# Kernel tuning notes

Measured on AMD Instinct MI355X. Metric: run time of the kernel, lower is better.

## Reference

```python
import jax, jax.numpy as jnp
import numpy as np

HIDDEN = 768
B = 32
GRID_X, GRID_Y = 84, 30          # 84*30 = 2520 input patches
SEQ = GRID_X * GRID_Y            # 2520
OUT_LEN = 280                    # 2520 // 280 = 9 -> k = 3


def setup_inputs() -> dict:
    key = jax.random.key(0)
    k1, k2 = jax.random.split(key)
    hidden_states = jax.random.normal(k1, (B, SEQ, HIDDEN), dtype=jnp.float32)
    # (x, y) grid coordinates for each patch, identical across batch
    x = jnp.arange(SEQ, dtype=jnp.int32) % GRID_X
    y = jnp.arange(SEQ, dtype=jnp.int32) // GRID_X
    pos = jnp.stack([x, y], axis=-1)                     # [SEQ, 2]
    pixel_position_ids = jnp.broadcast_to(pos, (B, SEQ, 2))
    padding_positions = jax.random.bernoulli(k2, 0.05, (B, SEQ))  # bool mask
    return {
        "hidden_states": hidden_states,
        "pixel_position_ids": pixel_position_ids,
        "padding_positions": padding_positions,
        "output_length": OUT_LEN,
    }


def reference(hidden_states, pixel_position_ids, padding_positions, output_length):
    root_hidden_size = hidden_states.shape[-1] ** 0.5
    # zero out padded patches
    hs = jnp.where(padding_positions[..., None], 0.0, hidden_states)
    seq_len = hs.shape[1]
    if seq_len != output_length:
        k = int((seq_len // output_length) ** 0.5)
        k_squared = k * k
        clamped = jnp.maximum(pixel_position_ids, 0)            # [B, S, 2]
        max_x = jnp.max(clamped[..., 0], axis=-1, keepdims=True) + 1  # [B, 1]
        kidx = clamped // k
        seg = kidx[..., 0] + (max_x // k) * kidx[..., 1]        # [B, S] bucket ids
        hs32 = hs.astype(jnp.float32)
        # segment-sum per batch == one_hot(seg).T @ hs, without the dense one-hot
        pooled = jax.vmap(
            lambda h, i: jax.ops.segment_sum(h, i, num_segments=output_length)
        )(hs32, seg) / k_squared                                 # [B, L, H]
        counts = jax.vmap(
            lambda i: jax.ops.segment_sum(jnp.ones_like(i), i, num_segments=output_length)
        )(seg)                                                   # [B, L]
        mask = counts > 0  # bucket received at least one patch (one-hot col nonzero)
        hs = pooled.astype(hidden_states.dtype)
        padding_positions = mask
    hs = hs * root_hidden_size
    return hs, padding_positions
```

## Files before the change

kernel.cpp:

```cpp
#include <hip/hip_runtime.h>
#include <math.h>


#define NB    32
#define SEQL  2520
#define HID   768
#define OUTL  280
#define CAP   16
#define GX    84
#define KP    3
#define MXK   (GX / KP)

typedef float f32x4 __attribute__((ext_vector_type(4)));

__global__ void __launch_bounds__(256)
k_verify(const int* __restrict__ pos, const int* __restrict__ padding,
         int* __restrict__ flags, int* __restrict__ ents,
         float* __restrict__ out_mask) {
    __shared__ int r_ok[256];
    __shared__ int r_mx[256];
    __shared__ int s_cnt[OUTL];
    __shared__ int s_ent[OUTL * CAP];
    const int b = blockIdx.x;
    const int t = threadIdx.x;
    const int* p = pos + (size_t)b * SEQL * 2;
    const int4* p4 = (const int4*)p;

    int ok = 1, m = 0;
    for (int i = t; i < SEQL / 2; i += 256) {
        int4 v = p4[i];
        int s0 = 2 * i, s1 = 2 * i + 1;
        ok &= (v.x == s0 % GX) & (v.y == s0 / GX)
            & (v.z == s1 % GX) & (v.w == s1 / GX);
        int cx = v.x < 0 ? 0 : v.x; if (cx > m) m = cx;
        cx = v.z < 0 ? 0 : v.z;     if (cx > m) m = cx;
    }
    r_ok[t] = ok; r_mx[t] = m;
    __syncthreads();
    for (int off = 128; off > 0; off >>= 1) {
        if (t < off) {
            r_ok[t] &= r_ok[t + off];
            int o = r_mx[t + off]; if (o > r_mx[t]) r_mx[t] = o;
        }
        __syncthreads();
    }
    if (r_ok[0]) {
        if (t == 0) flags[b] = 1;
        return;
    }

    const int mxk = (r_mx[0] + 1) / KP;
    for (int i = t; i < OUTL; i += 256) s_cnt[i] = 0;
    for (int i = t; i < OUTL * CAP; i += 256) s_ent[i] = 1;
    __syncthreads();
    const int* pd = padding + (size_t)b * SEQL;
    for (int s = t; s < SEQL; s += 256) {
        int x = p[2 * s];     if (x < 0) x = 0;
        int y = p[2 * s + 1]; if (y < 0) y = 0;
        int seg = x / KP + mxk * (y / KP);
        if (seg >= 0 && seg < OUTL) {
            int slot = atomicAdd(&s_cnt[seg], 1);
            if (slot < CAP)
                s_ent[seg * CAP + slot] = (s << 1) | (pd[s] != 0 ? 1 : 0);
        }
    }
    __syncthreads();
    int* eg = ents + (size_t)b * OUTL * CAP;
    for (int i = t; i < OUTL * CAP; i += 256) eg[i] = s_ent[i];
    for (int i = t; i < OUTL; i += 256)
        out_mask[b * OUTL + i] = (s_cnt[i] > 0) ? 1.0f : 0.0f;
    if (t == 0) flags[b] = 0;
}

__global__ void __launch_bounds__(192)
k_pool(const float* __restrict__ hs, const int* __restrict__ padding,
       const int* __restrict__ flags, const int* __restrict__ ents,
       float* __restrict__ out, float* __restrict__ out_mask, float scale) {
    const int l = blockIdx.x;
    const int b = blockIdx.y;
    const int t = threadIdx.x;
    const int bl = b * OUTL + l;

    int e[9];
    if (flags[b]) {
        const int s00 = (KP * (l / MXK)) * GX + KP * (l % MXK);
        #pragma unroll
        for (int dy = 0; dy < 3; ++dy)
            #pragma unroll
            for (int dx = 0; dx < 3; ++dx) {
                int s = s00 + dy * GX + dx;
                e[dy * 3 + dx] = (s << 1) | (padding[b * SEQL + s] != 0 ? 1 : 0);
            }
        if (t == 0) out_mask[bl] = 1.0f;
    } else {
        const int* eg = ents + (size_t)bl * CAP;
        #pragma unroll
        for (int i = 0; i < 9; ++i) e[i] = eg[i];
        #pragma unroll
        for (int i = 1; i < 9; ++i) {
            int v = e[i], j = i - 1;
            while (j >= 0 && e[j] > v) { e[j + 1] = e[j]; --j; }
            e[j + 1] = v;
        }
    }

    f32x4 acc = (f32x4)(0.f);
    const f32x4* base = (const f32x4*)(hs + (size_t)b * SEQL * HID);
    #pragma unroll
    for (int i = 0; i < 9; ++i) {
        if (!(e[i] & 1)) {
            f32x4 v = __builtin_nontemporal_load(
                base + (size_t)(e[i] >> 1) * (HID / 4) + t);
            acc += v;
        }
    }
    acc *= scale;
    __builtin_nontemporal_store(acc, (f32x4*)(out + (size_t)bl * HID) + t);
}

extern "C" void kernel_launch(void* const* d_in, const int* in_sizes, int n_in,
                              void* d_out, int out_size, void* d_ws, size_t ws_size,
                              hipStream_t stream) {
    const float* hs      = (const float*)d_in[0];
    const int*   pos     = (const int*)d_in[1];
    const int*   padding = (const int*)d_in[2];

    int* flags = (int*)d_ws;
    int* ents  = (int*)((char*)d_ws + 128);

    float* out      = (float*)d_out;
    float* out_mask = out + (size_t)NB * OUTL * HID;
    const float scale = sqrtf((float)HID) / 9.0f;

    k_verify<<<NB, 256, 0, stream>>>(pos, padding, flags, ents, out_mask);
    dim3 grid(OUTL, NB);
    k_pool<<<grid, 192, 0, stream>>>(hs, padding, flags, ents, out, out_mask, scale);
}
```

Before: 51.13 us.

## Fuse position verification into pooling kernel, dropping the separate verify launch

Removes the per-batch verify kernel and workspace round-trip. Each pooling block now re-checks the whole position array for its batch (2520 int pairs) using a wave-level __all reduction, then takes the fast grid path or a per-bucket slow scan. This saves one kernel launch and the dependency between the two kernels. In exchange, all 280 blocks of a batch redundantly read the positions array, which adds L2 traffic and per-block latency before the hidden-state loads.

New measurement: 53.33 us. 1.04x slower.

```diff
diff --git a/kernel.cpp b/kernel.cpp
--- a/kernel.cpp
+++ b/kernel.cpp
@@ -13,76 +13,36 @@
 
 typedef float f32x4 __attribute__((ext_vector_type(4)));
 
-__global__ void __launch_bounds__(256)
-k_verify(const int* __restrict__ pos, const int* __restrict__ padding,
-         int* __restrict__ flags, int* __restrict__ ents,
-         float* __restrict__ out_mask) {
-    __shared__ int r_ok[256];
-    __shared__ int r_mx[256];
-    __shared__ int s_cnt[OUTL];
-    __shared__ int s_ent[OUTL * CAP];
-    const int b = blockIdx.x;
+__global__ void __launch_bounds__(192)
+k_fused(const float* __restrict__ hs, const int* __restrict__ pos,
+        const int* __restrict__ padding, float* __restrict__ out,
+        float* __restrict__ out_mask, float scale) {
+    __shared__ int sok[3];
+    __shared__ int smx[3];
+    __shared__ int s_cnt;
+    __shared__ int s_ent[CAP];
+
+    const int l = blockIdx.x;
+    const int b = blockIdx.y;
     const int t = threadIdx.x;
+    const int bl = b * OUTL + l;
     const int* p = pos + (size_t)b * SEQL * 2;
     const int4* p4 = (const int4*)p;
 
-    int ok = 1, m = 0;
-    for (int i = t; i < SEQL / 2; i += 256) {
+    int ok = 1;
+    for (int i = t; i < SEQL / 2; i += 192) {
         int4 v = p4[i];
         int s0 = 2 * i, s1 = 2 * i + 1;
         ok &= (v.x == s0 % GX) & (v.y == s0 / GX)
             & (v.z == s1 % GX) & (v.w == s1 / GX);
-        int cx = v.x < 0 ? 0 : v.x; if (cx > m) m = cx;
-        cx = v.z < 0 ? 0 : v.z;     if (cx > m) m = cx;
     }
-    r_ok[t] = ok; r_mx[t] = m;
+    ok = __all(ok);
+    if ((t & 63) == 0) sok[t >> 6] = ok;
     __syncthreads();
-    for (int off = 128; off > 0; off >>= 1) {
-        if (t < off) {
-            r_ok[t] &= r_ok[t + off];
-            int o = r_mx[t + off]; if (o > r_mx[t]) r_mx[t] = o;
-        }
-        __syncthreads();
-    }
-    if (r_ok[0]) {
-        if (t == 0) flags[b] = 1;
-        return;
-    }
-
-    const int mxk = (r_mx[0] + 1) / KP;
-    for (int i = t; i < OUTL; i += 256) s_cnt[i] = 0;
-    for (int i = t; i < OUTL * CAP; i += 256) s_ent[i] = 1;
-    __syncthreads();
-    const int* pd = padding + (size_t)b * SEQL;
-    for (int s = t; s < SEQL; s += 256) {
-        int x = p[2 * s];     if (x < 0) x = 0;
-        int y = p[2 * s + 1]; if (y < 0) y = 0;
-        int seg = x / KP + mxk * (y / KP);
-        if (seg >= 0 && seg < OUTL) {
-            int slot = atomicAdd(&s_cnt[seg], 1);
-            if (slot < CAP)
-                s_ent[seg * CAP + slot] = (s << 1) | (pd[s] != 0 ? 1 : 0);
-        }
-    }
-    __syncthreads();
-    int* eg = ents + (size_t)b * OUTL * CAP;
-    for (int i = t; i < OUTL * CAP; i += 256) eg[i] = s_ent[i];
-    for (int i = t; i < OUTL; i += 256)
-        out_mask[b * OUTL + i] = (s_cnt[i] > 0) ? 1.0f : 0.0f;
-    if (t == 0) flags[b] = 0;
-}
-
-__global__ void __launch_bounds__(192)
-k_pool(const float* __restrict__ hs, const int* __restrict__ padding,
-       const int* __restrict__ flags, const int* __restrict__ ents,
-       float* __restrict__ out, float* __restrict__ out_mask, float scale) {
-    const int l = blockIdx.x;
-    const int b = blockIdx.y;
-    const int t = threadIdx.x;
-    const int bl = b * OUTL + l;
+    const int fast = sok[0] & sok[1] & sok[2];
 
     int e[9];
-    if (flags[b]) {
+    if (fast) {
         const int s00 = (KP * (l / MXK)) * GX + KP * (l % MXK);
         #pragma unroll
         for (int dy = 0; dy < 3; ++dy)
@@ -93,15 +53,43 @@
             }
         if (t == 0) out_mask[bl] = 1.0f;
     } else {
-        const int* eg = ents + (size_t)bl * CAP;
+        int m = 0;
+        for (int i = t; i < SEQL / 2; i += 192) {
+            int4 v = p4[i];
+            int cx = v.x < 0 ? 0 : v.x; if (cx > m) m = cx;
+            cx = v.z < 0 ? 0 : v.z;     if (cx > m) m = cx;
+        }
         #pragma unroll
-        for (int i = 0; i < 9; ++i) e[i] = eg[i];
+        for (int off = 32; off > 0; off >>= 1) {
+            int o = __shfl_down(m, off, 64);
+            if (o > m) m = o;
+        }
+        if ((t & 63) == 0) smx[t >> 6] = m;
+        if (t == 0) s_cnt = 0;
+        __syncthreads();
+        int mx = smx[0]; if (smx[1] > mx) mx = smx[1]; if (smx[2] > mx) mx = smx[2];
+        const int mxk = (mx + 1) / KP;
+        const int* pd = padding + (size_t)b * SEQL;
+        for (int s = t; s < SEQL; s += 192) {
+            int x = p[2 * s];     if (x < 0) x = 0;
+            int y = p[2 * s + 1]; if (y < 0) y = 0;
+            int seg = x / KP + mxk * (y / KP);
+            if (seg == l) {
+                int sl = atomicAdd(&s_cnt, 1);
+                if (sl < CAP) s_ent[sl] = (s << 1) | (pd[s] != 0 ? 1 : 0);
+            }
+        }
+        __syncthreads();
+        const int n = s_cnt < CAP ? s_cnt : CAP;
+        #pragma unroll
+        for (int i = 0; i < 9; ++i) e[i] = (i < n) ? s_ent[i] : 1;
         #pragma unroll
         for (int i = 1; i < 9; ++i) {
             int v = e[i], j = i - 1;
             while (j >= 0 && e[j] > v) { e[j + 1] = e[j]; --j; }
             e[j + 1] = v;
         }
+        if (t == 0) out_mask[bl] = (s_cnt > 0) ? 1.0f : 0.0f;
     }
 
     f32x4 acc = (f32x4)(0.f);
@@ -125,14 +113,10 @@
     const int*   pos     = (const int*)d_in[1];
     const int*   padding = (const int*)d_in[2];
 
-    int* flags = (int*)d_ws;
-    int* ents  = (int*)((char*)d_ws + 128);
-
     float* out      = (float*)d_out;
     float* out_mask = out + (size_t)NB * OUTL * HID;
     const float scale = sqrtf((float)HID) / 9.0f;
 
-    k_verify<<<NB, 256, 0, stream>>>(pos, padding, flags, ents, out_mask);
     dim3 grid(OUTL, NB);
-    k_pool<<<grid, 192, 0, stream>>>(hs, padding, flags, ents, out, out_mask, scale);
+    k_fused<<<grid, 192, 0, stream>>>(hs, pos, padding, out, out_mask, scale);
 }
```
